# Kernel optimization log

Measured on AMD Instinct MI355X. Metric: run time of the kernel, lower is better.

The kernel has to match this reference:

```python
import jax, jax.numpy as jnp
import numpy as np

B, T, C = 4, 2048, 2048
N_HEAD, N_KV = 16, 4
HD = C // N_HEAD          # 128
N_REP = N_HEAD // N_KV    # 4


def setup_inputs() -> dict:
    key = jax.random.key(0)
    k1, k2, k3 = jax.random.split(key, 3)
    x = jax.random.normal(k1, (B, T, C), dtype=jnp.float32)
    # RoPE frequencies: complex freqs_cis stored as [T, HD//2, 2] = (cos, sin)
    inv_freq = 1.0 / (10000.0 ** (jnp.arange(0, HD, 2, dtype=jnp.float32) / HD))  # [HD//2]
    angles = jnp.arange(T, dtype=jnp.float32)[:, None] * inv_freq[None, :]        # [T, HD//2]
    freqs_cis = jnp.stack([jnp.cos(angles), jnp.sin(angles)], axis=-1)            # [T, HD//2, 2]
    w_qkv = jax.random.normal(k2, (C, (N_HEAD + 2 * N_KV) * HD), dtype=jnp.float32) * 0.02
    w_proj = jax.random.normal(k3, (C, C), dtype=jnp.float32) * 0.02
    return {"x": x, "freqs_cis": freqs_cis, "w_qkv": w_qkv, "w_proj": w_proj}


def _apply_rope(t, freqs_cis):
    # t: [B, T, H, HD]; pairs (even, odd) along last dim form complex numbers
    shp = t.shape
    t2 = t.astype(jnp.float32).reshape(*shp[:-1], HD // 2, 2)
    cos = freqs_cis[None, :, None, :, 0]  # [1, T, 1, HD//2]
    sin = freqs_cis[None, :, None, :, 1]
    re = t2[..., 0] * cos - t2[..., 1] * sin
    im = t2[..., 0] * sin + t2[..., 1] * cos
    return jnp.stack([re, im], axis=-1).reshape(shp).astype(t.dtype)


def reference(x, freqs_cis, w_qkv, w_proj):
    Bs, Ts, Cs = x.shape
    qkv = x @ w_qkv  # [B, T, (H+2KV)*HD]
    q, k, v = jnp.split(qkv, [N_HEAD * HD, N_HEAD * HD + N_KV * HD], axis=-1)
    q = q.reshape(Bs, Ts, N_HEAD, HD)
    k = k.reshape(Bs, Ts, N_KV, HD)
    v = v.reshape(Bs, Ts, N_KV, HD)
    q = _apply_rope(q, freqs_cis)
    k = _apply_rope(k, freqs_cis)
    # GQA attention without materializing repeated k/v: group query heads per kv head
    qg = q.reshape(Bs, Ts, N_KV, N_REP, HD)
    scale = 1.0 / jnp.sqrt(jnp.asarray(HD, dtype=jnp.float32))
    scores = jnp.einsum('btkrd,bskd->bkrts', qg, k) * scale  # [B, KV, REP, T, T]
    att = jax.nn.softmax(scores.astype(jnp.float32), axis=-1).astype(q.dtype)
    y = jnp.einsum('bkrts,bskd->btkrd', att, v).reshape(Bs, Ts, Cs)
    return y @ w_proj
```

## Files before the change

kernel.cpp:

```cpp
#include <hip/hip_runtime.h>

using u16 = unsigned short;
using u32 = unsigned int;
typedef float f32x4 __attribute__((ext_vector_type(4)));
typedef float f32x16 __attribute__((ext_vector_type(16)));
typedef short s16x8 __attribute__((ext_vector_type(8)));
typedef unsigned int u32x4 __attribute__((ext_vector_type(4)));

__device__ __forceinline__ u16 f2bf(float x) {
  u32 u = __float_as_uint(x);
  u += 0x7fffu + ((u >> 16) & 1u);
  return (u16)(u >> 16);
}
__device__ __forceinline__ u32 pack2bf(float lo, float hi) {
  return (u32)f2bf(lo) | ((u32)f2bf(hi) << 16);
}
__device__ __forceinline__ float bf2f(u16 v) {
  return __uint_as_float(((u32)v) << 16);
}
__device__ __forceinline__ u32 cvtpk(float lo, float hi) {
  u32 r;
  asm("v_cvt_pk_bf16_f32 %0, %1, %2" : "=v"(r) : "v"(lo), "v"(hi));
  return r;
}
__device__ __forceinline__ void plswap(u32& a, u32& b) {
  asm volatile("v_permlane32_swap_b32 %0, %1" : "+v"(a), "+v"(b));
}
__device__ __forceinline__ void gload16(const u16* g, u16* l) {
  __builtin_amdgcn_global_load_lds(
      (__attribute__((address_space(1))) void*)(u16*)g,
      (__attribute__((address_space(3))) void*)l, 16, 0, 0);
}
__device__ __forceinline__ f32x4 fzero4() {
  f32x4 v = {0.f, 0.f, 0.f, 0.f};
  return v;
}
__device__ __forceinline__ f32x16 fzero16() {
  f32x16 v = {0, 0, 0, 0, 0, 0, 0, 0, 0, 0, 0, 0, 0, 0, 0, 0};
  return v;
}

__global__ __launch_bounds__(256) void k_convert(const float* __restrict__ in,
                                                 u16* __restrict__ out, int n8) {
  int i = blockIdx.x * 256 + threadIdx.x;
  if (i >= n8) return;
  const float4* p = (const float4*)in;
  float4 a = p[2 * i], b = p[2 * i + 1];
  uint4 o;
  o.x = pack2bf(a.x, a.y);
  o.y = pack2bf(a.z, a.w);
  o.z = pack2bf(b.x, b.y);
  o.w = pack2bf(b.z, b.w);
  ((uint4*)out)[i] = o;
}

__global__ __launch_bounds__(256) void k_transpose(const float* __restrict__ w,
                                                   u16* __restrict__ wt, int N, int K) {
  __shared__ float tile[64][65];
  int n0 = blockIdx.x * 64, k0 = blockIdx.y * 64;
  int tid = threadIdx.x;
  int rr = tid >> 6, cc = tid & 63;
#pragma unroll
  for (int p = 0; p < 16; ++p)
    tile[p * 4 + rr][cc] = w[(size_t)(k0 + p * 4 + rr) * N + n0 + cc];
  __syncthreads();
#pragma unroll
  for (int p = 0; p < 16; ++p)
    wt[(size_t)(n0 + p * 4 + rr) * K + k0 + cc] = f2bf(tile[cc][p * 4 + rr]);
}

template <bool OBF>
__global__ __launch_bounds__(256) void k_gemm_bt(const u16* __restrict__ A,
                                                 const u16* __restrict__ Bt,
                                                 void* __restrict__ Out, int Nd, int Kd) {
  __shared__ u16 As[2][128 * 32];
  __shared__ u16 Bs[2][128 * 32];
  u32 bid = blockIdx.x, nwg = gridDim.x;
  u32 wgid = (bid & 7) * (nwg >> 3) + (bid >> 3);
  int ntn = Nd >> 7;
  int bm = wgid / ntn, bn = wgid % ntn;
  int tid = threadIdx.x, w = tid >> 6, lane = tid & 63;
  int wm = w >> 1, wn = w & 1;
  int lg = lane >> 4, lq = lane & 15;

  const u16* a0 = A + (size_t)(bm * 128 + w * 32 + (lane >> 2)) * Kd + (lane & 3) * 8;
  const u16* a1 = a0 + (size_t)16 * Kd;
  const u16* b0 = Bt + (size_t)(bn * 128 + w * 32 + (lane >> 2)) * Kd + (lane & 3) * 8;
  const u16* b1 = b0 + (size_t)16 * Kd;

  auto stage = [&](int buf, int k0) {
    gload16(a0 + k0, &As[buf][w * 1024]);
    gload16(a1 + k0, &As[buf][w * 1024 + 512]);
    gload16(b0 + k0, &Bs[buf][w * 1024]);
    gload16(b1 + k0, &Bs[buf][w * 1024 + 512]);
  };

  f32x4 acc[4][4];
#pragma unroll
  for (int m = 0; m < 4; ++m)
#pragma unroll
    for (int n = 0; n < 4; ++n) acc[m][n] = fzero4();

  int nk = Kd >> 5;
  stage(0, 0);
  __syncthreads();
  for (int t = 0; t < nk; ++t) {
    int cur = t & 1;
    if (t + 1 < nk) stage(cur ^ 1, (t + 1) << 5);
    s16x8 af[4], bfr[4];
#pragma unroll
    for (int m = 0; m < 4; ++m)
      af[m] = *(const s16x8*)&As[cur][(wm * 64 + m * 16 + lq) * 32 + lg * 8];
#pragma unroll
    for (int n = 0; n < 4; ++n)
      bfr[n] = *(const s16x8*)&Bs[cur][(wn * 64 + n * 16 + lq) * 32 + lg * 8];
#pragma unroll
    for (int m = 0; m < 4; ++m)
#pragma unroll
      for (int n = 0; n < 4; ++n)
        acc[m][n] = __builtin_amdgcn_mfma_f32_16x16x32_bf16(af[m], bfr[n], acc[m][n], 0, 0, 0);
    __syncthreads();
  }

  int r0 = bm * 128 + wm * 64, c0 = bn * 128 + wn * 64;
  if (OBF) {
    u16* O = (u16*)Out;
#pragma unroll
    for (int m = 0; m < 4; ++m)
#pragma unroll
      for (int n = 0; n < 4; ++n)
#pragma unroll
        for (int r = 0; r < 4; ++r)
          O[(size_t)(r0 + m * 16 + lg * 4 + r) * Nd + c0 + n * 16 + lq] = f2bf(acc[m][n][r]);
  } else {
    float* O = (float*)Out;
#pragma unroll
    for (int m = 0; m < 4; ++m)
#pragma unroll
      for (int n = 0; n < 4; ++n)
#pragma unroll
        for (int r = 0; r < 4; ++r)
          O[(size_t)(r0 + m * 16 + lg * 4 + r) * Nd + c0 + n * 16 + lq] = acc[m][n][r];
  }
}

__device__ __forceinline__ u32 rope_pair(short a, short b, float c, float s, float sc) {
  float x0 = bf2f((u16)a), x1 = bf2f((u16)b);
  return pack2bf((x0 * c - x1 * s) * sc, (x0 * s + x1 * c) * sc);
}

__global__ __launch_bounds__(256) void k_rope_scatter(const u16* __restrict__ qkv,
                                                      const float* __restrict__ fr,
                                                      u16* __restrict__ Q, u16* __restrict__ K,
                                                      u16* __restrict__ Vt) {
  int idx = blockIdx.x * 256 + threadIdx.x;
  if (idx >= 8192 * 384) return;
  int row = idx / 384, g = idx % 384;
  int b = row >> 11, t = row & 2047;
  int col = g * 8;
  const u16* src = qkv + (size_t)row * 3072 + col;
  if (col < 2560) {
    int isq = col < 2048;
    float sc = isq ? 0.127517432f : 1.0f;
    int c2 = isq ? col : col - 2048;
    int h = c2 >> 7, d = c2 & 127;
    u16* dst = isq ? (Q + ((size_t)(b * 16 + h) * 2048 + t) * 128 + d)
                   : (K + ((size_t)(b * 4 + h) * 2048 + t) * 128 + d);
    const float4* fp = (const float4*)(fr + (size_t)t * 128 + d);
    float4 f01 = fp[0], f23 = fp[1];
    s16x8 v = *(const s16x8*)src;
    uint4 o;
    o.x = rope_pair(v[0], v[1], f01.x, f01.y, sc);
    o.y = rope_pair(v[2], v[3], f01.z, f01.w, sc);
    o.z = rope_pair(v[4], v[5], f23.x, f23.y, sc);
    o.w = rope_pair(v[6], v[7], f23.z, f23.w, sc);
    *(uint4*)dst = o;
  } else {
    int c2 = col - 2560;
    int h = c2 >> 7, d = c2 & 127;
    s16x8 v = *(const s16x8*)src;
    u16* base = Vt + ((size_t)(b * 4 + h) * 128 + d) * 2048 + t;
#pragma unroll
    for (int j = 0; j < 8; ++j) base[(size_t)j * 2048] = (u16)v[j];
  }
}

__global__ __launch_bounds__(256, 2) void k_attn(const u16* __restrict__ Qg,
                                                 const u16* __restrict__ Kg,
                                                 const u16* __restrict__ Vg,
                                                 u16* __restrict__ Yg) {
  __shared__ u16 Kl[2][64 * 128];
  __shared__ u16 Vl[2][128 * 64];
  u32 bid = blockIdx.x;
  u32 wgid = (bid & 7) * 128 + (bid >> 3);
  int qt = wgid & 15, bh = wgid >> 4;
  int b = bh >> 4, h = bh & 15, kvh = h >> 2;
  int tid = threadIdx.x, w = tid >> 6, lane = tid & 63;
  int l31 = lane & 31, hi = lane >> 5;
  const u16* Qb = Qg + ((size_t)bh * 2048 + qt * 128 + w * 32 + l31) * 128;
  const u16* Kb = Kg + (size_t)(b * 4 + kvh) * 2048 * 128;
  const u16* Vb = Vg + (size_t)(b * 4 + kvh) * 128 * 2048;

  s16x8 qf[8];
#pragma unroll
  for (int kc = 0; kc < 8; ++kc)
    qf[kc] = *(const s16x8*)(Qb + kc * 16 + hi * 8);

  f32x16 o[4];
#pragma unroll
  for (int i = 0; i < 4; ++i) o[i] = fzero16();
  float l_run = 0.f;

  int krow4 = lane >> 4;
  int kc_ = lane & 15;
  int vrow8 = lane >> 3;
  int vc_ = lane & 7;

  auto stageK = [&](int buf, int key0) {
#pragma unroll
    for (int i = 0; i < 4; ++i) {
      int key = w * 16 + i * 4 + krow4;
      gload16(Kb + (size_t)(key0 + key) * 128 + ((kc_ ^ (key & 15)) * 8),
              &Kl[buf][(w * 16 + i * 4) * 128]);
    }
  };
  auto stageV = [&](int buf, int key0) {
#pragma unroll
    for (int i = 0; i < 4; ++i) {
      int d = w * 32 + i * 8 + vrow8;
      gload16(Vb + (size_t)d * 2048 + key0 + ((vc_ ^ (d & 7)) * 8),
              &Vl[buf][(w * 32 + i * 8) * 64]);
    }
  };

  stageK(0, 0);
  stageV(0, 0);
  __syncthreads();

  for (int kt = 0; kt < 32; ++kt) {
    int cur = kt & 1;
    if (kt < 31) {
      stageK(cur ^ 1, (kt + 1) * 64);
      stageV(cur ^ 1, (kt + 1) * 64);
    }

    f32x16 s0 = fzero16(), s1 = fzero16();
    int swz = l31 & 15;
    __builtin_amdgcn_s_setprio(1);
#pragma unroll
    for (int kc = 0; kc < 8; ++kc) {
      int slot = (kc * 2 + hi) ^ swz;
      s16x8 a0 = *(const s16x8*)&Kl[cur][l31 * 128 + slot * 8];
      s0 = __builtin_amdgcn_mfma_f32_32x32x16_bf16(a0, qf[kc], s0, 0, 0, 0);
      s16x8 a1 = *(const s16x8*)&Kl[cur][(32 + l31) * 128 + slot * 8];
      s1 = __builtin_amdgcn_mfma_f32_32x32x16_bf16(a1, qf[kc], s1, 0, 0, 0);
    }
    __builtin_amdgcn_s_setprio(0);

    u32 pw[16];
    float ps = 0.f;
    auto sm_half = [&](const f32x16& sv, u32* pwg) {
#pragma unroll
      for (int g = 0; g < 2; ++g) {
        float p[8];
#pragma unroll
        for (int j = 0; j < 8; ++j) p[j] = exp2f(sv[g * 8 + j]);
        ps += ((p[0] + p[1]) + (p[2] + p[3])) + ((p[4] + p[5]) + (p[6] + p[7]));
        u32 x0 = cvtpk(p[0], p[1]), y0 = cvtpk(p[4], p[5]);
        u32 x1 = cvtpk(p[2], p[3]), y1 = cvtpk(p[6], p[7]);
        plswap(x0, y0);
        plswap(x1, y1);
        pwg[g * 4 + 0] = x0;
        pwg[g * 4 + 1] = x1;
        pwg[g * 4 + 2] = y0;
        pwg[g * 4 + 3] = y1;
      }
    };
    sm_half(s0, pw);
    sm_half(s1, pw + 8);
    l_run += ps;

    __builtin_amdgcn_s_setprio(1);
#pragma unroll
    for (int g = 0; g < 4; ++g) {
      u32x4 t;
      t.x = pw[g * 4 + 0];
      t.y = pw[g * 4 + 1];
      t.z = pw[g * 4 + 2];
      t.w = pw[g * 4 + 3];
      s16x8 pf = __builtin_bit_cast(s16x8, t);
#pragma unroll
      for (int df = 0; df < 4; ++df) {
        int idx = (df * 32 + l31) * 64 + (((g * 2 + hi) ^ (l31 & 7)) * 8);
        s16x8 vf = *(const s16x8*)&Vl[cur][idx];
        o[df] = __builtin_amdgcn_mfma_f32_32x32x16_bf16(vf, pf, o[df], 0, 0, 0);
      }
    }
    __builtin_amdgcn_s_setprio(0);

    __syncthreads();
  }

  l_run += __shfl_xor(l_run, 32);
  float inv = 1.0f / l_run;
  int q = qt * 128 + w * 32 + l31;
  u16* yr = Yg + ((size_t)(b * 2048) + q) * 2048 + h * 128;
#pragma unroll
  for (int df = 0; df < 4; ++df)
#pragma unroll
    for (int q4 = 0; q4 < 4; ++q4) {
      int d0 = df * 32 + q4 * 8 + hi * 4;
      uint2 vv;
      vv.x = cvtpk(o[df][q4 * 4 + 0] * inv, o[df][q4 * 4 + 1] * inv);
      vv.y = cvtpk(o[df][q4 * 4 + 2] * inv, o[df][q4 * 4 + 3] * inv);
      *(uint2*)&yr[d0] = vv;
    }
}

extern "C" void kernel_launch(void* const* d_in, const int* in_sizes, int n_in,
                              void* d_out, int out_size, void* d_ws, size_t ws_size,
                              hipStream_t stream) {
  const float* x = (const float*)d_in[0];
  const float* fr = (const float*)d_in[1];
  const float* wqkv = (const float*)d_in[2];
  const float* wproj = (const float*)d_in[3];
  char* ws = (char*)d_ws;
  u16* xbf = (u16*)(ws + 0);
  u16* wqkvT = (u16*)(ws + 33554432);
  u16* wprojT = (u16*)(ws + 46137344);
  u16* qkv = (u16*)(ws + 54525952);
  u16* Qb = (u16*)(ws + 104857600);
  u16* Kb = (u16*)(ws + 138412032);
  u16* Vtb = (u16*)(ws + 146800640);

  k_convert<<<8192, 256, 0, stream>>>(x, xbf, 8192 * 2048 / 8);
  k_transpose<<<dim3(48, 32), 256, 0, stream>>>(wqkv, wqkvT, 3072, 2048);
  k_transpose<<<dim3(32, 32), 256, 0, stream>>>(wproj, wprojT, 2048, 2048);
  k_gemm_bt<true><<<64 * 24, 256, 0, stream>>>(xbf, wqkvT, qkv, 3072, 2048);
  k_rope_scatter<<<12288, 256, 0, stream>>>(qkv, fr, Qb, Kb, Vtb);
  k_attn<<<1024, 256, 0, stream>>>(Qb, Kb, Vtb, xbf);
  k_gemm_bt<false><<<64 * 16, 256, 0, stream>>>(xbf, wprojT, d_out, 2048, 2048);
}
```

Before: 424.5 us.

## Replace GEMM with 256x256-tile 8-wave pipelined kernel and reswizzle attention V staging

Replaces the 128x128 double-buffered GEMM with a 512-thread, 256x256-tile kernel. It splits each K=64 step into four MFMA quadrants interleaved with LDS reads, global_load_lds prefetch two steps ahead, explicit waitcnt and hard barriers. A/B tiles use a paired-row XOR swizzle layout to reduce LDS bank conflicts and raise compute per loaded byte. The attention kernel's V staging is changed to the same 128-element-row swizzle with precomputed offsets. The trade-offs are more registers and LDS per block, more barriers per step, and fewer blocks, with 256 or 384 total.

```diff
diff --git a/kernel.cpp b/kernel.cpp
--- a/kernel.cpp
+++ b/kernel.cpp
@@ -38,6 +38,11 @@
 __device__ __forceinline__ f32x16 fzero16() {
   f32x16 v = {0, 0, 0, 0, 0, 0, 0, 0, 0, 0, 0, 0, 0, 0, 0, 0};
   return v;
+}
+__device__ __forceinline__ void barrier_hard() {
+  __builtin_amdgcn_sched_barrier(0);
+  __builtin_amdgcn_s_barrier();
+  __builtin_amdgcn_sched_barrier(0);
 }
 
 __global__ __launch_bounds__(256) void k_convert(const float* __restrict__ in,
@@ -70,77 +75,168 @@
 }
 
 template <bool OBF>
-__global__ __launch_bounds__(256) void k_gemm_bt(const u16* __restrict__ A,
-                                                 const u16* __restrict__ Bt,
-                                                 void* __restrict__ Out, int Nd, int Kd) {
-  __shared__ u16 As[2][128 * 32];
-  __shared__ u16 Bs[2][128 * 32];
+__global__ __launch_bounds__(512, 2) void k_gemm8(const u16* __restrict__ A,
+                                                  const u16* __restrict__ Bt,
+                                                  void* __restrict__ Out, int Nd, int Kd) {
+  __shared__ u16 Al[2][2][8192];
+  __shared__ u16 Bl[2][2][8192];
   u32 bid = blockIdx.x, nwg = gridDim.x;
   u32 wgid = (bid & 7) * (nwg >> 3) + (bid >> 3);
-  int ntn = Nd >> 7;
+  int ntn = Nd >> 8;
   int bm = wgid / ntn, bn = wgid % ntn;
   int tid = threadIdx.x, w = tid >> 6, lane = tid & 63;
-  int wm = w >> 1, wn = w & 1;
-  int lg = lane >> 4, lq = lane & 15;
-
-  const u16* a0 = A + (size_t)(bm * 128 + w * 32 + (lane >> 2)) * Kd + (lane & 3) * 8;
-  const u16* a1 = a0 + (size_t)16 * Kd;
-  const u16* b0 = Bt + (size_t)(bn * 128 + w * 32 + (lane >> 2)) * Kd + (lane & 3) * 8;
-  const u16* b1 = b0 + (size_t)16 * Kd;
-
-  auto stage = [&](int buf, int k0) {
-    gload16(a0 + k0, &As[buf][w * 1024]);
-    gload16(a1 + k0, &As[buf][w * 1024 + 512]);
-    gload16(b0 + k0, &Bs[buf][w * 1024]);
-    gload16(b1 + k0, &Bs[buf][w * 1024 + 512]);
-  };
-
-  f32x4 acc[4][4];
-#pragma unroll
-  for (int m = 0; m < 4; ++m)
+  int wm = w >> 2, wn = w & 3;
+  int lq = lane & 15, lg = lane >> 4;
+
+  const u16* Ab = A + (size_t)(bm * 256) * Kd;
+  const u16* Bb = Bt + (size_t)(bn * 256) * Kd;
+
+  u32 offA[2][2], offB[2][2];
+#pragma unroll
+  for (int set = 0; set < 2; ++set)
+#pragma unroll
+    for (int inst = 0; inst < 2; ++inst) {
+      int c = inst * 512 + tid;
+      int ldsrow = c >> 4, sl = c & 15;
+      int orig = sl ^ (ldsrow & 15);
+      int pr = ldsrow * 2 + (orig >> 3);
+      int kch = orig & 7;
+      int rA = (pr & 63) + ((pr >> 6) & 1) * 128 + set * 64;
+      int rB = (pr & 31) + (pr >> 5) * 64 + set * 32;
+      offA[set][inst] = (u32)(rA * Kd + kch * 8);
+      offB[set][inst] = (u32)(rB * Kd + kch * 8);
+    }
+
+  int aoff[4][2], boff[4][2];
+#pragma unroll
+  for (int mf = 0; mf < 4; ++mf)
+#pragma unroll
+    for (int kk = 0; kk < 2; ++kk) {
+      int pr = wm * 64 + mf * 16 + lq;
+      int slot = (((pr & 1) << 3) + kk * 4 + lg) ^ ((pr >> 1) & 15);
+      aoff[mf][kk] = (pr >> 1) * 128 + slot * 8;
+    }
+#pragma unroll
+  for (int nf = 0; nf < 4; ++nf)
+#pragma unroll
+    for (int kk = 0; kk < 2; ++kk) {
+      int pr = wn * 32 + (nf & 1) * 16 + lq;
+      int slot = (((pr & 1) << 3) + kk * 4 + lg) ^ ((pr >> 1) & 15);
+      boff[nf][kk] = (pr >> 1) * 128 + slot * 8;
+    }
+
+  int ldsbase = w * 512;
+
+  auto stgA = [&](int dbuf, int set, int u) {
+    const u16* s = Ab + u * 64;
+    gload16(s + offA[set][0], &Al[dbuf][set][ldsbase]);
+    gload16(s + offA[set][1], &Al[dbuf][set][4096 + ldsbase]);
+  };
+  auto stgB = [&](int dbuf, int set, int u) {
+    const u16* s = Bb + u * 64;
+    gload16(s + offB[set][0], &Bl[dbuf][set][ldsbase]);
+    gload16(s + offB[set][1], &Bl[dbuf][set][4096 + ldsbase]);
+  };
+
+  f32x4 acc[8][4];
+#pragma unroll
+  for (int m = 0; m < 8; ++m)
 #pragma unroll
     for (int n = 0; n < 4; ++n) acc[m][n] = fzero4();
 
-  int nk = Kd >> 5;
-  stage(0, 0);
-  __syncthreads();
-  for (int t = 0; t < nk; ++t) {
-    int cur = t & 1;
-    if (t + 1 < nk) stage(cur ^ 1, (t + 1) << 5);
-    s16x8 af[4], bfr[4];
-#pragma unroll
-    for (int m = 0; m < 4; ++m)
-      af[m] = *(const s16x8*)&As[cur][(wm * 64 + m * 16 + lq) * 32 + lg * 8];
-#pragma unroll
-    for (int n = 0; n < 4; ++n)
-      bfr[n] = *(const s16x8*)&Bs[cur][(wn * 64 + n * 16 + lq) * 32 + lg * 8];
-#pragma unroll
-    for (int m = 0; m < 4; ++m)
-#pragma unroll
-      for (int n = 0; n < 4; ++n)
-        acc[m][n] = __builtin_amdgcn_mfma_f32_16x16x32_bf16(af[m], bfr[n], acc[m][n], 0, 0, 0);
-    __syncthreads();
+  s16x8 af[4][2], bf[4][2];
+
+  auto LDA = [&](int dbuf, int set) {
+#pragma unroll
+    for (int mf = 0; mf < 4; ++mf)
+#pragma unroll
+      for (int kk = 0; kk < 2; ++kk)
+        af[mf][kk] = *(const s16x8*)&Al[dbuf][set][aoff[mf][kk]];
+  };
+  auto LDB = [&](int dbuf, int nf0) {
+#pragma unroll
+    for (int nf = 0; nf < 2; ++nf)
+#pragma unroll
+      for (int kk = 0; kk < 2; ++kk)
+        bf[nf0 + nf][kk] = *(const s16x8*)&Bl[dbuf][nf0 >> 1][boff[nf0 + nf][kk]];
+  };
+  auto DO_MFMA = [&](int mb, int nb) {
+    __builtin_amdgcn_s_setprio(1);
+#pragma unroll
+    for (int mf = 0; mf < 4; ++mf)
+#pragma unroll
+      for (int nf = 0; nf < 2; ++nf)
+#pragma unroll
+        for (int kk = 0; kk < 2; ++kk)
+          acc[mb + mf][nb + nf] = __builtin_amdgcn_mfma_f32_16x16x32_bf16(
+              af[mf][kk], bf[nb + nf][kk], acc[mb + mf][nb + nf], 0, 0, 0);
+    __builtin_amdgcn_s_setprio(0);
+  };
+  auto LGKM0 = [&]() {
+    asm volatile("s_waitcnt lgkmcnt(0)" ::: "memory");
+    __builtin_amdgcn_sched_barrier(0);
+  };
+
+  int nt = Kd >> 6;
+  stgA(0, 0, 0); stgB(0, 0, 0); stgA(0, 1, 0); stgB(0, 1, 0);
+  stgA(1, 0, 1); stgB(1, 1, 1); stgA(1, 1, 1);
+  asm volatile("s_waitcnt vmcnt(6)" ::: "memory");
+  barrier_hard();
+
+  for (int u = 0; u < nt; ++u) {
+    int c = u & 1, nc = c ^ 1;
+    bool g1 = (u + 1 < nt), g2 = (u + 2 < nt);
+    LDA(c, 0);
+    LDB(c, 0);
+    if (g1) stgB(nc, 0, u + 1);
+    barrier_hard();
+    LGKM0();
+    DO_MFMA(0, 0);
+    barrier_hard();
+    LDB(c, 2);
+    if (g2) stgA(c, 0, u + 2);
+    barrier_hard();
+    LGKM0();
+    DO_MFMA(0, 2);
+    barrier_hard();
+    LDA(c, 1);
+    if (g2) stgB(c, 1, u + 2);
+    barrier_hard();
+    LGKM0();
+    DO_MFMA(4, 2);
+    barrier_hard();
+    if (g2) stgA(c, 1, u + 2);
+    barrier_hard();
+    DO_MFMA(4, 0);
+    if (g2) {
+      asm volatile("s_waitcnt vmcnt(6)" ::: "memory");
+    } else {
+      asm volatile("s_waitcnt vmcnt(0)" ::: "memory");
+    }
+    barrier_hard();
   }
 
-  int r0 = bm * 128 + wm * 64, c0 = bn * 128 + wn * 64;
+  int r0 = bm * 256 + wm * 128, c0 = bn * 256 + wn * 64;
   if (OBF) {
     u16* O = (u16*)Out;
 #pragma unroll
-    for (int m = 0; m < 4; ++m)
-#pragma unroll
-      for (int n = 0; n < 4; ++n)
+    for (int mf = 0; mf < 8; ++mf)
+#pragma unroll
+      for (int nf = 0; nf < 4; ++nf)
 #pragma unroll
         for (int r = 0; r < 4; ++r)
-          O[(size_t)(r0 + m * 16 + lg * 4 + r) * Nd + c0 + n * 16 + lq] = f2bf(acc[m][n][r]);
+          O[(size_t)(r0 + mf * 16 + lg * 4 + r) * Nd + c0 + nf * 16 + lq] =
+              f2bf(acc[mf][nf][r]);
   } else {
     float* O = (float*)Out;
 #pragma unroll
-    for (int m = 0; m < 4; ++m)
-#pragma unroll
-      for (int n = 0; n < 4; ++n)
+    for (int mf = 0; mf < 8; ++mf)
+#pragma unroll
+      for (int nf = 0; nf < 4; ++nf)
 #pragma unroll
         for (int r = 0; r < 4; ++r)
-          O[(size_t)(r0 + m * 16 + lg * 4 + r) * Nd + c0 + n * 16 + lq] = acc[m][n][r];
+          O[(size_t)(r0 + mf * 16 + lg * 4 + r) * Nd + c0 + nf * 16 + lq] =
+              acc[mf][nf][r];
   }
 }
 
@@ -190,7 +286,7 @@
                                                  const u16* __restrict__ Vg,
                                                  u16* __restrict__ Yg) {
   __shared__ u16 Kl[2][64 * 128];
-  __shared__ u16 Vl[2][128 * 64];
+  __shared__ u16 Vl[2][64 * 128];
   u32 bid = blockIdx.x;
   u32 wgid = (bid & 7) * 128 + (bid >> 3);
   int qt = wgid & 15, bh = wgid >> 4;
@@ -213,8 +309,16 @@
 
   int krow4 = lane >> 4;
   int kc_ = lane & 15;
-  int vrow8 = lane >> 3;
-  int vc_ = lane & 7;
+  u32 offV[4];
+#pragma unroll
+  for (int i = 0; i < 4; ++i) {
+    int c = i * 256 + tid;
+    int ldsrow = c >> 4, sl = c & 15;
+    int orig = sl ^ (ldsrow & 15);
+    int d = ldsrow * 2 + (orig >> 3);
+    int kch = orig & 7;
+    offV[i] = (u32)(d * 2048 + kch * 8);
+  }
 
   auto stageK = [&](int buf, int key0) {
 #pragma unroll
@@ -226,11 +330,8 @@
   };
   auto stageV = [&](int buf, int key0) {
 #pragma unroll
-    for (int i = 0; i < 4; ++i) {
-      int d = w * 32 + i * 8 + vrow8;
-      gload16(Vb + (size_t)d * 2048 + key0 + ((vc_ ^ (d & 7)) * 8),
-              &Vl[buf][(w * 32 + i * 8) * 64]);
-    }
+    for (int i = 0; i < 4; ++i)
+      gload16(Vb + key0 + offV[i], &Vl[buf][(i * 256 + w * 64) * 8]);
   };
 
   stageK(0, 0);
@@ -291,8 +392,9 @@
       s16x8 pf = __builtin_bit_cast(s16x8, t);
 #pragma unroll
       for (int df = 0; df < 4; ++df) {
-        int idx = (df * 32 + l31) * 64 + (((g * 2 + hi) ^ (l31 & 7)) * 8);
-        s16x8 vf = *(const s16x8*)&Vl[cur][idx];
+        int d = df * 32 + l31;
+        int slot = (((d & 1) << 3) + g * 2 + hi) ^ ((d >> 1) & 15);
+        s16x8 vf = *(const s16x8*)&Vl[cur][(d >> 1) * 128 + slot * 8];
         o[df] = __builtin_amdgcn_mfma_f32_32x32x16_bf16(vf, pf, o[df], 0, 0, 0);
       }
     }
@@ -336,8 +438,8 @@
   k_convert<<<8192, 256, 0, stream>>>(x, xbf, 8192 * 2048 / 8);
   k_transpose<<<dim3(48, 32), 256, 0, stream>>>(wqkv, wqkvT, 3072, 2048);
   k_transpose<<<dim3(32, 32), 256, 0, stream>>>(wproj, wprojT, 2048, 2048);
-  k_gemm_bt<true><<<64 * 24, 256, 0, stream>>>(xbf, wqkvT, qkv, 3072, 2048);
+  k_gemm8<true><<<32 * 12, 512, 0, stream>>>(xbf, wqkvT, qkv, 3072, 2048);
   k_rope_scatter<<<12288, 256, 0, stream>>>(qkv, fr, Qb, Kb, Vtb);
   k_attn<<<1024, 256, 0, stream>>>(Qb, Kb, Vtb, xbf);
-  k_gemm_bt<false><<<64 * 16, 256, 0, stream>>>(xbf, wprojT, d_out, 2048, 2048);
-}
+  k_gemm8<false><<<32 * 8, 512, 0, stream>>>(xbf, wprojT, d_out, 2048, 2048);
+}
```

Result: faster. 409.8 us (-3.5%).
